# Performance work log

Hardware: AMD Instinct MI355X
Metric: run time of the kernel (lower is better)

Reference implementation:

```python
import jax, jax.numpy as jnp
import numpy as np

NEG = -1000.0  # fill value for unmatched (type_mask != ti) entries

B, N, R = 4, 48, 16
T = 2 * R + 1          # 33 transition channels
Nc, L = 80, 3          # chains, chain length
Nt, Ni = 16, 5         # triples, chains per triple (uniform c_sections)


def setup_inputs() -> dict:
    key = jax.random.key(0)
    k1, k2, k3, k4, k5 = jax.random.split(key, 5)
    transitions = jax.random.normal(k1, (B, N, N, T), dtype=jnp.float32)
    type_mask = jax.random.randint(k2, (B, N, N, R), 0, 2, dtype=jnp.int32)
    rules = jax.random.randint(k3, (Nc, L), 0, T, dtype=jnp.int32)
    # stacked per-triple weights [Nt, Ni] (orig: ParameterList of [Ni,1]) and biases [Nt]
    weights = jax.random.normal(k4, (Nt, Ni), dtype=jnp.float32) / np.sqrt(Ni)
    biases = jax.random.uniform(k5, (Nt,), dtype=jnp.float32, minval=-1.0, maxval=1.0)
    return {"transitions": transitions, "type_mask": type_mask, "rules": rules,
            "weights": weights, "biases": biases}


def path_scores(transitions, rules):
    """Tropical (max-plus) chain DP.
    transitions: [B,N,N,T], rules: [Nc,L] -> scores [B,N,N,Nc]
    scores[b,x,y,c] = max over intermediate nodes of sum of hop scores.
    """
    Lc = rules.shape[1]
    hops = [transitions[..., rules[:, l]] for l in range(Lc)]  # each [B,N,N,Nc]
    # max-plus "matmul": s[b,x,y,c] = max_k hops0[b,x,k,c] + hops1[b,k,y,c]
    s = jnp.max(hops[0][:, :, :, None, :] + hops[1][:, None, :, :, :], axis=2)
    for l in range(2, Lc):
        s = jnp.max(s[:, :, :, None, :] + hops[l][:, None, :, :, :], axis=2)
    return s


def reference(transitions, type_mask, rules, weights, biases):
    # scores over all chains, exponentiated: [B,N,N,Nc]
    s = jnp.exp(path_scores(transitions, rules))
    # group chains by triple (uniform sections): [B,N,N,Nt,Ni]
    s = s.reshape(s.shape[0], s.shape[1], s.shape[2], Nt, Ni)
    # per-triple weighted sum + bias; one triple per relation so Nt == R
    comb = jnp.einsum('bxytc,tc->bxyt', s, weights) + biases  # [B,N,N,R]
    # masked_scatter: write score where type_mask[...,i] == ti (== 0 here), else -1000
    out = jnp.where(type_mask == 0, comb, NEG)
    return out
```

## Files before the change

kernel.cpp:

```cpp
#include <hip/hip_runtime.h>
#include <cmath>

#define BB 4
#define NN 48
#define PP (NN * NN)
#define TT 33
#define RR 16
#define NC 80
#define NI 5
#define NEG (-1000.0f)

#define XS 24
#define XP 25
#define NTH 384

__global__ __launch_bounds__(256) void transpose_kernel(
    const float* __restrict__ trans,
    float*       __restrict__ tpose)
{
    __shared__ float tile[64 * TT];
    const int blk = blockIdx.x;
    const int b   = blk / 36;
    const int p0  = (blk - b * 36) * 64;

    const float4* src = (const float4*)(trans + ((size_t)b * PP + p0) * TT);
    for (int j = threadIdx.x; j < 64 * TT / 4; j += 256)
        ((float4*)tile)[j] = src[j];
    __syncthreads();

    for (int j = threadIdx.x; j < TT * 64; j += 256) {
        const int t  = j >> 6;
        const int pl = j & 63;
        tpose[((size_t)b * TT + t) * PP + p0 + pl] = tile[pl * TT + t];
    }
}

__global__ __launch_bounds__(NTH) void fused_scorer(
    const float* __restrict__ tpose,
    const int*   __restrict__ rules,
    const float* __restrict__ weights,
    const float* __restrict__ biases,
    const int*   __restrict__ mask,
    float*       __restrict__ out)
{
    __shared__ float H0T[NN * XP];
    __shared__ float H1 [PP];
    __shared__ float H2 [PP];
    __shared__ float S1T[NN * XP];

    const int blk = blockIdx.x;
    const int xh  = blk & 1;
    const int bt  = blk >> 1;
    const int b   = bt >> 4;
    const int t   = bt & 15;
    const int xbase = xh * XS;

    const int xl = threadIdx.x >> 4;
    const int yt = threadIdx.x & 15;
    const int y0 = yt * 3;

    float acc_out[3] = {0.0f, 0.0f, 0.0f};

    for (int ci = 0; ci < NI; ++ci) {
        const int c  = t * NI + ci;
        const int r0 = rules[c * 3 + 0];
        const int r1 = rules[c * 3 + 1];
        const int r2 = rules[c * 3 + 2];
        const float w = weights[c];

        const float* p0 = tpose + ((size_t)b * TT + r0) * PP + xbase * NN;
        const float* p1 = tpose + ((size_t)b * TT + r1) * PP;
        const float* p2 = tpose + ((size_t)b * TT + r2) * PP;

        __syncthreads();

        for (int j = threadIdx.x; j < PP / 4; j += NTH) {
            ((float4*)H1)[j] = ((const float4*)p1)[j];
            ((float4*)H2)[j] = ((const float4*)p2)[j];
        }
        for (int j = threadIdx.x; j < XS * NN / 4; j += NTH) {
            const float4 v0 = ((const float4*)p0)[j];
            const int x = (4 * j) / NN;
            const int k = (4 * j) - x * NN;
            H0T[(k + 0) * XP + x] = v0.x;
            H0T[(k + 1) * XP + x] = v0.y;
            H0T[(k + 2) * XP + x] = v0.z;
            H0T[(k + 3) * XP + x] = v0.w;
        }
        __syncthreads();

        float a0 = -INFINITY, a1 = -INFINITY, a2 = -INFINITY;
        #pragma unroll 4
        for (int kp = 0; kp < NN / 2; ++kp) {
            const int k = kp * 2;
            const float h0 = H0T[k * XP + xl];
            const float h1 = H0T[(k + 1) * XP + xl];
            a0 = fmaxf(a0, fmaxf(h0 + H1[k * NN + y0 + 0], h1 + H1[(k + 1) * NN + y0 + 0]));
            a1 = fmaxf(a1, fmaxf(h0 + H1[k * NN + y0 + 1], h1 + H1[(k + 1) * NN + y0 + 1]));
            a2 = fmaxf(a2, fmaxf(h0 + H1[k * NN + y0 + 2], h1 + H1[(k + 1) * NN + y0 + 2]));
        }
        S1T[(y0 + 0) * XP + xl] = a0;
        S1T[(y0 + 1) * XP + xl] = a1;
        S1T[(y0 + 2) * XP + xl] = a2;
        __syncthreads();

        float s0 = -INFINITY, s1 = -INFINITY, s2 = -INFINITY;
        #pragma unroll 4
        for (int kp = 0; kp < NN / 2; ++kp) {
            const int k = kp * 2;
            const float h0 = S1T[k * XP + xl];
            const float h1 = S1T[(k + 1) * XP + xl];
            s0 = fmaxf(s0, fmaxf(h0 + H2[k * NN + y0 + 0], h1 + H2[(k + 1) * NN + y0 + 0]));
            s1 = fmaxf(s1, fmaxf(h0 + H2[k * NN + y0 + 1], h1 + H2[(k + 1) * NN + y0 + 1]));
            s2 = fmaxf(s2, fmaxf(h0 + H2[k * NN + y0 + 2], h1 + H2[(k + 1) * NN + y0 + 2]));
        }
        acc_out[0] += w * __expf(s0);
        acc_out[1] += w * __expf(s1);
        acc_out[2] += w * __expf(s2);
    }

    const float bias = biases[t];
    const int xg = xbase + xl;
    #pragma unroll
    for (int j = 0; j < 3; ++j) {
        const size_t oidx = ((size_t)(b * PP + xg * NN + y0 + j)) * RR + t;
        out[oidx] = (mask[oidx] == 0) ? (acc_out[j] + bias) : NEG;
    }
}

extern "C" void kernel_launch(void* const* d_in, const int* in_sizes, int n_in,
                              void* d_out, int out_size, void* d_ws, size_t ws_size,
                              hipStream_t stream)
{
    const float* trans   = (const float*)d_in[0];
    const int*   mask    = (const int*)  d_in[1];
    const int*   rules   = (const int*)  d_in[2];
    const float* weights = (const float*)d_in[3];
    const float* biases  = (const float*)d_in[4];
    float* out = (float*)d_out;

    float* tpose = (float*)d_ws;

    transpose_kernel<<<BB * 36, 256, 0, stream>>>(trans, tpose);

    fused_scorer<<<BB * RR * 2, NTH, 0, stream>>>(tpose, rules, weights,
                                                  biases, mask, out);
}
```

Before: 83.02 us.

## Drop transpose kernel, gather channels directly and split x into quarters

```diff
diff --git a/kernel.cpp b/kernel.cpp
--- a/kernel.cpp
+++ b/kernel.cpp
@@ -10,33 +10,12 @@
 #define NI 5
 #define NEG (-1000.0f)
 
-#define XS 24
-#define XP 25
-#define NTH 384
-
-__global__ __launch_bounds__(256) void transpose_kernel(
-    const float* __restrict__ trans,
-    float*       __restrict__ tpose)
-{
-    __shared__ float tile[64 * TT];
-    const int blk = blockIdx.x;
-    const int b   = blk / 36;
-    const int p0  = (blk - b * 36) * 64;
-
-    const float4* src = (const float4*)(trans + ((size_t)b * PP + p0) * TT);
-    for (int j = threadIdx.x; j < 64 * TT / 4; j += 256)
-        ((float4*)tile)[j] = src[j];
-    __syncthreads();
-
-    for (int j = threadIdx.x; j < TT * 64; j += 256) {
-        const int t  = j >> 6;
-        const int pl = j & 63;
-        tpose[((size_t)b * TT + t) * PP + p0 + pl] = tile[pl * TT + t];
-    }
-}
+#define XS 12
+#define XP 13
+#define NTH 192
 
 __global__ __launch_bounds__(NTH) void fused_scorer(
-    const float* __restrict__ tpose,
+    const float* __restrict__ trans,
     const int*   __restrict__ rules,
     const float* __restrict__ weights,
     const float* __restrict__ biases,
@@ -49,15 +28,17 @@
     __shared__ float S1T[NN * XP];
 
     const int blk = blockIdx.x;
-    const int xh  = blk & 1;
-    const int bt  = blk >> 1;
+    const int xq  = blk & 3;
+    const int bt  = blk >> 2;
     const int b   = bt >> 4;
     const int t   = bt & 15;
-    const int xbase = xh * XS;
+    const int xbase = xq * XS;
 
     const int xl = threadIdx.x >> 4;
     const int yt = threadIdx.x & 15;
     const int y0 = yt * 3;
+
+    const float* tb = trans + (size_t)b * PP * TT;
 
     float acc_out[3] = {0.0f, 0.0f, 0.0f};
 
@@ -68,24 +49,17 @@
         const int r2 = rules[c * 3 + 2];
         const float w = weights[c];
 
-        const float* p0 = tpose + ((size_t)b * TT + r0) * PP + xbase * NN;
-        const float* p1 = tpose + ((size_t)b * TT + r1) * PP;
-        const float* p2 = tpose + ((size_t)b * TT + r2) * PP;
-
         __syncthreads();
 
-        for (int j = threadIdx.x; j < PP / 4; j += NTH) {
-            ((float4*)H1)[j] = ((const float4*)p1)[j];
-            ((float4*)H2)[j] = ((const float4*)p2)[j];
+        for (int i = threadIdx.x; i < PP; i += NTH) {
+            const size_t base = (size_t)i * TT;
+            H1[i] = tb[base + r1];
+            H2[i] = tb[base + r2];
         }
-        for (int j = threadIdx.x; j < XS * NN / 4; j += NTH) {
-            const float4 v0 = ((const float4*)p0)[j];
-            const int x = (4 * j) / NN;
-            const int k = (4 * j) - x * NN;
-            H0T[(k + 0) * XP + x] = v0.x;
-            H0T[(k + 1) * XP + x] = v0.y;
-            H0T[(k + 2) * XP + x] = v0.z;
-            H0T[(k + 3) * XP + x] = v0.w;
+        for (int i = threadIdx.x; i < XS * NN; i += NTH) {
+            const int xls = i / NN;
+            const int k   = i - xls * NN;
+            H0T[k * XP + xls] = tb[(size_t)((xbase + xls) * NN + k) * TT + r0];
         }
         __syncthreads();
 
@@ -138,11 +112,8 @@
     const float* weights = (const float*)d_in[3];
     const float* biases  = (const float*)d_in[4];
     float* out = (float*)d_out;
+    (void)d_ws; (void)ws_size;
 
-    float* tpose = (float*)d_ws;
-
-    transpose_kernel<<<BB * 36, 256, 0, stream>>>(trans, tpose);
-
-    fused_scorer<<<BB * RR * 2, NTH, 0, stream>>>(tpose, rules, weights,
+    fused_scorer<<<BB * RR * 4, NTH, 0, stream>>>(trans, rules, weights,
                                                   biases, mask, out);
 }
```

New measurement: 89.74 us. +8.1%, slower.
